# Performance work log

Hardware: AMD Instinct MI355X
Metric: run time of the kernel (lower is better)

The kernel has to match this reference:

```python
import jax, jax.numpy as jnp
import numpy as np

N_NODES = 1_000_000
N_EDGES = 16_000_000
N_FEAT = 128
NUM_GRAPHS = 8192


def setup_inputs() -> dict:
    key = jax.random.key(0)
    k_x, k_e, k_b, k_w, k_pw, k_pb = jax.random.split(key, 6)
    x = jax.random.normal(k_x, (N_NODES, N_FEAT), dtype=jnp.float32)
    edge_index = jax.random.randint(k_e, (2, N_EDGES), 0, N_NODES, dtype=jnp.int64)
    batch = jnp.sort(jax.random.randint(k_b, (N_NODES,), 0, NUM_GRAPHS, dtype=jnp.int64))
    # GCNConv lin weight (F -> 1, no bias), xavier-ish scale
    W = jax.random.normal(k_w, (N_FEAT, 1), dtype=jnp.float32) * (6.0 / (N_FEAT + 1)) ** 0.5
    # post_pool Linear(1, 1, bias=True)
    pp_w = jax.random.normal(k_pw, (1, 1), dtype=jnp.float32)
    pp_b = jax.random.normal(k_pb, (1,), dtype=jnp.float32) * 0.1
    return {"x": x, "W": W, "pp_w": pp_w, "pp_b": pp_b,
            "edge_index": edge_index, "batch": batch}


def reference(x, W, pp_w, pp_b, edge_index, batch):
    N = x.shape[0]
    h = x @ W  # [N, 1] — tiny feature after GCNConv projection
    # add self-loops (PyG GCNConv default)
    loops = jnp.arange(N, dtype=edge_index.dtype)
    src = jnp.concatenate([edge_index[0], loops])  # message sources (col j)
    dst = jnp.concatenate([edge_index[1], loops])  # aggregation targets (row i)
    # symmetric degree normalization: deg over targets incl. self-loops
    deg = jax.ops.segment_sum(jnp.ones(src.shape[0], dtype=h.dtype), dst,
                              num_segments=N)
    dinv = jnp.where(deg > 0, jax.lax.rsqrt(deg), 0.0)
    norm = dinv[src] * dinv[dst]  # [E+N]
    # gather -> normalize -> scatter-add
    agg = jax.ops.segment_sum(norm[:, None] * h[src], dst, num_segments=N)  # [N,1]
    # global_add_pool by graph id
    pooled = jax.ops.segment_sum(agg, batch, num_segments=NUM_GRAPHS)  # [G,1]
    return pooled @ pp_w.T + pp_b  # Linear(1,1)
```

## Files before the change

kernel.cpp:

```cpp
#include <hip/hip_runtime.h>
#include <hip/hip_fp16.h>

#define NUM_GRAPHS 8192
#define BSHIFT 12
#define BSIZE 4096
#define CHUNK 4096
#define NGRP 32
#define REPL 8
#define WINDOW 256
#define WPAD 257
#define FNT 512

__global__ void __launch_bounds__(256)
pair_scatter_kernel(const int* __restrict__ src, const int* __restrict__ dst,
                    int E, int nchunks, int NBUK, int capG,
                    unsigned* __restrict__ cursor, unsigned* __restrict__ slab) {
    __shared__ unsigned cnt[256];
    __shared__ unsigned lbase[256];
    __shared__ unsigned sbase[256];
    __shared__ unsigned staged[CHUNK];
    __shared__ unsigned char sbuck[CHUNK];
    __shared__ unsigned s_tot;

    const int4* s4 = (const int4*)src;
    const int4* d4 = (const int4*)dst;
    int E4 = E >> 2;
    int tid = threadIdx.x;
    int g = blockIdx.x & (NGRP - 1);

    for (int chunk = blockIdx.x; chunk < nchunks; chunk += gridDim.x) {
        cnt[tid] = 0; __syncthreads();
        int b4 = chunk * (CHUNK / 4);
        int4 vd[4], vs[4];
        unsigned short r[16];
        #pragma unroll
        for (int k = 0; k < 4; ++k) {
            int idx = b4 + k * 256 + tid;
            if (idx < E4) { vd[k] = d4[idx]; vs[k] = s4[idx]; }
            else          { vd[k] = make_int4(-1, -1, -1, -1); }
        }
        #pragma unroll
        for (int k = 0; k < 4; ++k) {
            if (vd[k].x >= 0) {
                r[4*k+0] = (unsigned short)atomicAdd(&cnt[vd[k].x >> BSHIFT], 1u);
                r[4*k+1] = (unsigned short)atomicAdd(&cnt[vd[k].y >> BSHIFT], 1u);
                r[4*k+2] = (unsigned short)atomicAdd(&cnt[vd[k].z >> BSHIFT], 1u);
                r[4*k+3] = (unsigned short)atomicAdd(&cnt[vd[k].w >> BSHIFT], 1u);
            }
        }
        __syncthreads();
        if (tid < 64) {
            unsigned run = 0;
            for (int c0 = 0; c0 < 256; c0 += 64) {
                unsigned v = cnt[c0 + tid];
                unsigned s = v;
                #pragma unroll
                for (int off = 1; off < 64; off <<= 1) {
                    unsigned o = __shfl_up(s, off);
                    if (tid >= off) s += o;
                }
                lbase[c0 + tid] = run + s - v;
                run += __shfl(s, 63);
            }
            if (tid == 0) s_tot = run;
        }
        if (tid < NBUK && cnt[tid])
            sbase[tid] = atomicAdd(&cursor[g * 256 + tid], cnt[tid]);
        __syncthreads();

        #pragma unroll
        for (int k = 0; k < 4; ++k) {
            if (vd[k].x >= 0) {
                int d0 = vd[k].x, d1 = vd[k].y, d2 = vd[k].z, d3 = vd[k].w;
                unsigned b0 = (unsigned)d0 >> BSHIFT, b1 = (unsigned)d1 >> BSHIFT;
                unsigned b2 = (unsigned)d2 >> BSHIFT, b3 = (unsigned)d3 >> BSHIFT;
                unsigned p0 = lbase[b0] + r[4*k+0];
                unsigned p1 = lbase[b1] + r[4*k+1];
                unsigned p2 = lbase[b2] + r[4*k+2];
                unsigned p3 = lbase[b3] + r[4*k+3];
                staged[p0] = ((unsigned)(d0 & (BSIZE-1)) << 20) | (unsigned)vs[k].x;
                staged[p1] = ((unsigned)(d1 & (BSIZE-1)) << 20) | (unsigned)vs[k].y;
                staged[p2] = ((unsigned)(d2 & (BSIZE-1)) << 20) | (unsigned)vs[k].z;
                staged[p3] = ((unsigned)(d3 & (BSIZE-1)) << 20) | (unsigned)vs[k].w;
                sbuck[p0] = (unsigned char)b0;
                sbuck[p1] = (unsigned char)b1;
                sbuck[p2] = (unsigned char)b2;
                sbuck[p3] = (unsigned char)b3;
            }
        }
        __syncthreads();
        unsigned tot = s_tot;
        for (unsigned pos = tid; pos < tot; pos += 256) {
            unsigned b = sbuck[pos];
            unsigned gp = sbase[b] + (pos - lbase[b]);
            if (gp < (unsigned)capG)
                slab[((size_t)g * NBUK + b) * capG + gp] = staged[pos];
        }
        __syncthreads();
    }
    if (blockIdx.x == 0 && tid < (E & 3)) {
        int i = (E & ~3) + tid;
        int d = dst[i];
        unsigned b = (unsigned)d >> BSHIFT;
        unsigned p = atomicAdd(&cursor[b], 1u);
        if (p < (unsigned)capG)
            slab[(size_t)b * capG + p] =
                ((unsigned)(d & (BSIZE-1)) << 20) | (unsigned)src[i];
    }
}

__global__ void __launch_bounds__(FNT)
hist_h_kernel(const unsigned* __restrict__ slab, int capG,
              const unsigned* __restrict__ cursor,
              unsigned* __restrict__ deg0, unsigned* __restrict__ deg1,
              const float* __restrict__ x, const float* __restrict__ W,
              float* __restrict__ h, int N, int NBUK, int nhblocks) {
    __shared__ unsigned hist[BSIZE];
    int bp = blockIdx.x, tid = threadIdx.x;

    if (bp < 2 * NBUK) {
        int b = bp >> 1, half = bp & 1;
        for (int t = tid; t < BSIZE; t += FNT) hist[t] = 0;
        __syncthreads();
        int g0 = half * 16;
        for (int gg = g0; gg < g0 + 16; gg += 8) {
            unsigned n[8], maxn = 0;
            const unsigned* sp[8];
            #pragma unroll
            for (int k = 0; k < 8; ++k) {
                unsigned nn = cursor[(gg + k) * 256 + b];
                if (nn > (unsigned)capG) nn = capG;
                n[k] = nn; if (nn > maxn) maxn = nn;
                sp[k] = slab + ((size_t)(gg + k) * NBUK + b) * capG;
            }
            for (unsigned i = tid; i < maxn; i += FNT) {
                unsigned e[8];
                #pragma unroll
                for (int k = 0; k < 8; ++k) e[k] = (i < n[k]) ? sp[k][i] : 0xFFFFFFFFu;
                #pragma unroll
                for (int k = 0; k < 8; ++k)
                    if (e[k] != 0xFFFFFFFFu) atomicAdd(&hist[e[k] >> 20], 1u);
            }
        }
        __syncthreads();
        int base = b << BSHIFT;
        int lim = N - base; if (lim > BSIZE) lim = BSIZE;
        unsigned* degP = half ? deg1 : deg0;
        for (int t = tid; t < lim; t += FNT) degP[base + t] = hist[t];
    } else {
        int hb = bp - 2 * NBUK;
        int gwave = (hb * FNT + tid) >> 6;
        int lane = tid & 63;
        int half = lane >> 5;
        int l32  = lane & 31;
        int total_waves = (nhblocks * FNT) >> 6;
        float4 wv = ((const float4*)W)[l32];
        for (int node = gwave * 2 + half; node < N; node += total_waves * 2) {
            float4 xv = ((const float4*)(x + (size_t)node * 128))[l32];
            float v = xv.x * wv.x + xv.y * wv.y + xv.z * wv.z + xv.w * wv.w;
            #pragma unroll
            for (int d = 16; d >= 1; d >>= 1) v += __shfl_xor(v, d);
            if (l32 == 0) h[node] = v;
        }
    }
}

__global__ void finalize_kernel(const float* __restrict__ h,
                                const unsigned* __restrict__ deg0,
                                const unsigned* __restrict__ deg1,
                                const int* __restrict__ batch,
                                unsigned short* __restrict__ hsh,
                                unsigned* __restrict__ pkw, int N) {
    int i = blockIdx.x * blockDim.x + threadIdx.x;
    int stride = gridDim.x * blockDim.x;
    for (; i < N; i += stride) {
        float di = rsqrtf((float)(deg0[i] + deg1[i] + 1u));
        hsh[i] = __half_as_ushort(__float2half(di * h[i]));
        pkw[i] = ((unsigned)batch[i] << 16) | __half_as_ushort(__float2half(di));
    }
}

__global__ void __launch_bounds__(512)
aggregate_kernel(const unsigned* __restrict__ slab, int capG,
                 const unsigned* __restrict__ cursor,
                 const unsigned* __restrict__ pkw,
                 const unsigned short* __restrict__ hsh,
                 float* __restrict__ pooled, int N, int NBUK) {
    __shared__ unsigned pkw_s[BSIZE];
    __shared__ float win[REPL * WPAD];
    int bp = blockIdx.x, tid = threadIdx.x;
    int b = bp >> 2, q = bp & 3;
    int base = b << BSHIFT;
    int lim = N - base; if (lim > BSIZE) lim = BSIZE;

    for (int t = tid; t < BSIZE; t += 512) pkw_s[t] = (t < lim) ? pkw[base + t] : 0u;
    for (int t = tid; t < REPL * WPAD; t += 512) win[t] = 0.0f;
    __syncthreads();
    int g_lo = (int)(pkw_s[0] >> 16);
    int g_hi = (lim > 0) ? (int)(pkw_s[lim - 1] >> 16) : g_lo;
    int width = g_hi - g_lo + 1;
    bool windowed = (width <= WINDOW);
    int r = tid & (REPL - 1);

    int n0 = q * (BSIZE / 4);
    int n1 = (q + 1) * (BSIZE / 4); if (n1 > lim) n1 = lim;
    for (int t = n0 + tid; t < n1; t += 512) {
        unsigned w = pkw_s[t];
        float di = __half2float(__ushort_as_half((unsigned short)(w & 0xFFFFu)));
        float c = di * __half2float(__ushort_as_half(hsh[base + t]));
        if (windowed) atomicAdd(&win[r * WPAD + ((w >> 16) - g_lo)], c);
        else          atomicAdd(&pooled[w >> 16], c);
    }

    int g0 = q * 8;
    unsigned n[8], maxn = 0;
    const unsigned* sp[8];
    #pragma unroll
    for (int k = 0; k < 8; ++k) {
        unsigned nn = cursor[(g0 + k) * 256 + b];
        if (nn > (unsigned)capG) nn = capG;
        n[k] = nn; if (nn > maxn) maxn = nn;
        sp[k] = slab + ((size_t)(g0 + k) * NBUK + b) * capG;
    }
    for (unsigned i = tid; i < maxn; i += 512) {
        unsigned e[8]; bool v[8];
        #pragma unroll
        for (int k = 0; k < 8; ++k) { v[k] = (i < n[k]); e[k] = v[k] ? sp[k][i] : 0u; }
        unsigned w[8];
        #pragma unroll
        for (int k = 0; k < 8; ++k) w[k] = pkw_s[e[k] >> 20];
        unsigned short hb[8];
        #pragma unroll
        for (int k = 0; k < 8; ++k) hb[k] = hsh[e[k] & 0xFFFFFu];
        #pragma unroll
        for (int k = 0; k < 8; ++k) {
            float hv = __half2float(__ushort_as_half(hb[k]));
            float di = __half2float(__ushort_as_half((unsigned short)(w[k] & 0xFFFFu)));
            float c = v[k] ? hv * di : 0.0f;
            if (windowed) atomicAdd(&win[r * WPAD + ((w[k] >> 16) - g_lo)], c);
            else if (v[k]) atomicAdd(&pooled[w[k] >> 16], c);
        }
    }
    __syncthreads();
    if (windowed) {
        for (int g = tid; g < width; g += 512) {
            float s = 0.0f;
            #pragma unroll
            for (int rr = 0; rr < REPL; ++rr) s += win[rr * WPAD + g];
            atomicAdd(&pooled[g_lo + g], s);
        }
    }
}

__global__ void out_kernel(const float* __restrict__ pooled,
                           const float* __restrict__ pp_w,
                           const float* __restrict__ pp_b,
                           float* __restrict__ out) {
    int g = blockIdx.x * blockDim.x + threadIdx.x;
    if (g < NUM_GRAPHS) out[g] = pooled[g] * pp_w[0] + pp_b[0];
}

__global__ void deg_atomic_kernel(const int* __restrict__ dst, int E,
                                  unsigned* __restrict__ deg) {
    int tid = blockIdx.x * blockDim.x + threadIdx.x;
    int stride = gridDim.x * blockDim.x;
    for (int i = tid; i < E; i += stride) atomicAdd(&deg[dst[i]], 1u);
}

__global__ void node_fb_kernel(const float* __restrict__ x,
                               const float* __restrict__ W,
                               const unsigned* __restrict__ deg,
                               const int* __restrict__ batch,
                               unsigned short* __restrict__ hsh,
                               unsigned* __restrict__ pkw, int N) {
    int gtid = blockIdx.x * blockDim.x + threadIdx.x;
    int wave = gtid >> 6;
    int lane = threadIdx.x & 63;
    int half = lane >> 5;
    int l32  = lane & 31;
    int node = wave * 2 + half;
    if (node >= N) return;
    float4 xv = ((const float4*)(x + (size_t)node * 128))[l32];
    float4 wv = ((const float4*)W)[l32];
    float v = xv.x * wv.x + xv.y * wv.y + xv.z * wv.z + xv.w * wv.w;
    #pragma unroll
    for (int d = 16; d >= 1; d >>= 1) v += __shfl_xor(v, d);
    if (l32 == 0) {
        float di = rsqrtf((float)(deg[node] + 1u));
        hsh[node] = __half_as_ushort(__float2half(di * v));
        pkw[node] = ((unsigned)batch[node] << 16) | __half_as_ushort(__float2half(di));
    }
}

__global__ void pool_self_fb_kernel(const unsigned short* __restrict__ hsh,
                                    const unsigned* __restrict__ pkw,
                                    float* __restrict__ pooled, int N) {
    int i = blockIdx.x * blockDim.x + threadIdx.x;
    if (i >= N) return;
    unsigned w = pkw[i];
    float di = __half2float(__ushort_as_half((unsigned short)(w & 0xFFFFu)));
    atomicAdd(&pooled[w >> 16], di * __half2float(__ushort_as_half(hsh[i])));
}

__global__ void __launch_bounds__(512)
edge_direct_kernel(const int* __restrict__ src, const int* __restrict__ dst, int E,
                   const unsigned short* __restrict__ hsh,
                   const unsigned* __restrict__ pkw,
                   float* __restrict__ pooled) {
    __shared__ float pool[NUM_GRAPHS];
    for (int g = threadIdx.x; g < NUM_GRAPHS; g += 512) pool[g] = 0.0f;
    __syncthreads();
    int tid = blockIdx.x * 512 + threadIdx.x;
    int stride = gridDim.x * 512;
    for (int i = tid; i < E; i += stride) {
        unsigned w = pkw[dst[i]];
        float c = __half2float(__ushort_as_half(hsh[src[i]])) *
                  __half2float(__ushort_as_half((unsigned short)(w & 0xFFFFu)));
        atomicAdd(&pool[w >> 16], c);
    }
    __syncthreads();
    for (int g = threadIdx.x; g < NUM_GRAPHS; g += 512)
        if (pool[g] != 0.0f) atomicAdd(&pooled[g], pool[g]);
}

extern "C" void kernel_launch(void* const* d_in, const int* in_sizes, int n_in,
                              void* d_out, int out_size, void* d_ws, size_t ws_size,
                              hipStream_t stream) {
    const float* x    = (const float*)d_in[0];
    const float* W    = (const float*)d_in[1];
    const float* pp_w = (const float*)d_in[2];
    const float* pp_b = (const float*)d_in[3];
    const int*   ei   = (const int*)d_in[4];
    const int*   batch= (const int*)d_in[5];
    float* out = (float*)d_out;

    const int E = in_sizes[4] / 2;
    const int N = in_sizes[5];
    const int* src = ei;
    const int* dst = ei + E;
    int NBUK = (N + BSIZE - 1) >> BSHIFT;
    int nchunks = (E + CHUNK - 1) / CHUNK;

    char* ws = (char*)d_ws;
    size_t off = 0;
    auto alloc = [&](size_t bytes) {
        size_t o = off; off = (off + bytes + 255) & ~(size_t)255; return o;
    };
    size_t zero_bytes = (size_t)NUM_GRAPHS * 4 + (size_t)NGRP * 256 * 4;
    size_t zero_off   = alloc(zero_bytes);
    float*    pooled = (float*)(ws + zero_off);
    unsigned* cursor = (unsigned*)(ws + zero_off + (size_t)NUM_GRAPHS * 4);

    size_t h_off    = alloc((size_t)N * 4);
    size_t deg0_off = alloc((size_t)N * 4);
    size_t deg1_off = alloc((size_t)N * 4);
    size_t hsh_off  = alloc((size_t)N * 2);
    size_t pkw_off  = alloc((size_t)N * 4);

    int meanG = E / (NBUK * NGRP) + 1;
    int capG = (meanG + meanG / 8 + 512 + 3) & ~3;
    size_t slab_off = alloc((size_t)NGRP * NBUK * (size_t)capG * 4);

    bool fast_ok = (NBUK <= 256) && (N <= (1 << 20)) && (off <= ws_size);

    float*          h    = (float*)(ws + h_off);
    unsigned*       deg0 = (unsigned*)(ws + deg0_off);
    unsigned*       deg1 = (unsigned*)(ws + deg1_off);
    unsigned short* hsh  = (unsigned short*)(ws + hsh_off);
    unsigned*       pkw  = (unsigned*)(ws + pkw_off);
    unsigned*       slab = (unsigned*)(ws + slab_off);

    hipMemsetAsync(ws + zero_off, 0, zero_bytes, stream);

    if (fast_ok) {
        int grid = nchunks < 4096 ? nchunks : 4096;
        pair_scatter_kernel<<<grid, 256, 0, stream>>>(src, dst, E, nchunks, NBUK,
                                                      capG, cursor, slab);
        int nhblocks = 2048;
        hist_h_kernel<<<2 * NBUK + nhblocks, FNT, 0, stream>>>(
            slab, capG, cursor, deg0, deg1, x, W, h, N, NBUK, nhblocks);
        finalize_kernel<<<1024, 256, 0, stream>>>(h, deg0, deg1, batch, hsh, pkw, N);
        aggregate_kernel<<<4 * NBUK, 512, 0, stream>>>(slab, capG, cursor, pkw,
                                                       hsh, pooled, N, NBUK);
    } else {
        hipMemsetAsync(deg0, 0, (size_t)N * 4, stream);
        deg_atomic_kernel<<<2048, 256, 0, stream>>>(dst, E, deg0);
        int node_blocks = (N + 7) / 8;
        node_fb_kernel<<<node_blocks, 256, 0, stream>>>(x, W, deg0, batch, hsh, pkw, N);
        pool_self_fb_kernel<<<(N + 255) / 256, 256, 0, stream>>>(hsh, pkw, pooled, N);
        edge_direct_kernel<<<512, 512, 0, stream>>>(src, dst, E, hsh, pkw, pooled);
    }

    out_kernel<<<(NUM_GRAPHS + 255) / 256, 256, 0, stream>>>(pooled, pp_w, pp_b, out);
}
```

Baseline: 276.2 us.

## Split h projection across scatter and histogram kernels to overlap memory work

The first half of the node projection h = x·W moves into the edge scatter kernel. Even block indices do the edge bucketing and odd ones compute h for the first N/2 nodes, and the histogram kernel now handles only the rest. The aim is to overlap the bandwidth-heavy read of x with the atomic-bound scatter, balancing the two kernels. The scatter grid falls from 4096 to 2048 blocks, which may lengthen the scatter phase.

```diff
diff --git a/kernel.cpp b/kernel.cpp
--- a/kernel.cpp
+++ b/kernel.cpp
@@ -10,11 +10,15 @@
 #define WINDOW 256
 #define WPAD 257
 #define FNT 512
+#define SGRID 2048
+#define HGRID1 2048
 
 __global__ void __launch_bounds__(256)
-pair_scatter_kernel(const int* __restrict__ src, const int* __restrict__ dst,
-                    int E, int nchunks, int NBUK, int capG,
-                    unsigned* __restrict__ cursor, unsigned* __restrict__ slab) {
+scatter_h_kernel(const int* __restrict__ src, const int* __restrict__ dst,
+                 int E, int nchunks, int NBUK, int capG,
+                 unsigned* __restrict__ cursor, unsigned* __restrict__ slab,
+                 const float* __restrict__ x, const float* __restrict__ W,
+                 float* __restrict__ h, int Nh) {
     __shared__ unsigned cnt[256];
     __shared__ unsigned lbase[256];
     __shared__ unsigned sbase[256];
@@ -22,90 +26,110 @@
     __shared__ unsigned char sbuck[CHUNK];
     __shared__ unsigned s_tot;
 
-    const int4* s4 = (const int4*)src;
-    const int4* d4 = (const int4*)dst;
-    int E4 = E >> 2;
+    int bid = blockIdx.x;
     int tid = threadIdx.x;
-    int g = blockIdx.x & (NGRP - 1);
-
-    for (int chunk = blockIdx.x; chunk < nchunks; chunk += gridDim.x) {
-        cnt[tid] = 0; __syncthreads();
-        int b4 = chunk * (CHUNK / 4);
-        int4 vd[4], vs[4];
-        unsigned short r[16];
-        #pragma unroll
-        for (int k = 0; k < 4; ++k) {
-            int idx = b4 + k * 256 + tid;
-            if (idx < E4) { vd[k] = d4[idx]; vs[k] = s4[idx]; }
-            else          { vd[k] = make_int4(-1, -1, -1, -1); }
-        }
-        #pragma unroll
-        for (int k = 0; k < 4; ++k) {
-            if (vd[k].x >= 0) {
-                r[4*k+0] = (unsigned short)atomicAdd(&cnt[vd[k].x >> BSHIFT], 1u);
-                r[4*k+1] = (unsigned short)atomicAdd(&cnt[vd[k].y >> BSHIFT], 1u);
-                r[4*k+2] = (unsigned short)atomicAdd(&cnt[vd[k].z >> BSHIFT], 1u);
-                r[4*k+3] = (unsigned short)atomicAdd(&cnt[vd[k].w >> BSHIFT], 1u);
-            }
-        }
-        __syncthreads();
-        if (tid < 64) {
-            unsigned run = 0;
-            for (int c0 = 0; c0 < 256; c0 += 64) {
-                unsigned v = cnt[c0 + tid];
-                unsigned s = v;
-                #pragma unroll
-                for (int off = 1; off < 64; off <<= 1) {
-                    unsigned o = __shfl_up(s, off);
-                    if (tid >= off) s += o;
+
+    if ((bid & 1) == 0) {
+        int sid = bid >> 1;
+        const int4* s4 = (const int4*)src;
+        const int4* d4 = (const int4*)dst;
+        int E4 = E >> 2;
+        int g = sid & (NGRP - 1);
+
+        for (int chunk = sid; chunk < nchunks; chunk += SGRID) {
+            cnt[tid] = 0; __syncthreads();
+            int b4 = chunk * (CHUNK / 4);
+            int4 vd[4], vs[4];
+            unsigned short r[16];
+            #pragma unroll
+            for (int k = 0; k < 4; ++k) {
+                int idx = b4 + k * 256 + tid;
+                if (idx < E4) { vd[k] = d4[idx]; vs[k] = s4[idx]; }
+                else          { vd[k] = make_int4(-1, -1, -1, -1); }
+            }
+            #pragma unroll
+            for (int k = 0; k < 4; ++k) {
+                if (vd[k].x >= 0) {
+                    r[4*k+0] = (unsigned short)atomicAdd(&cnt[vd[k].x >> BSHIFT], 1u);
+                    r[4*k+1] = (unsigned short)atomicAdd(&cnt[vd[k].y >> BSHIFT], 1u);
+                    r[4*k+2] = (unsigned short)atomicAdd(&cnt[vd[k].z >> BSHIFT], 1u);
+                    r[4*k+3] = (unsigned short)atomicAdd(&cnt[vd[k].w >> BSHIFT], 1u);
                 }
-                lbase[c0 + tid] = run + s - v;
-                run += __shfl(s, 63);
-            }
-            if (tid == 0) s_tot = run;
-        }
-        if (tid < NBUK && cnt[tid])
-            sbase[tid] = atomicAdd(&cursor[g * 256 + tid], cnt[tid]);
-        __syncthreads();
-
-        #pragma unroll
-        for (int k = 0; k < 4; ++k) {
-            if (vd[k].x >= 0) {
-                int d0 = vd[k].x, d1 = vd[k].y, d2 = vd[k].z, d3 = vd[k].w;
-                unsigned b0 = (unsigned)d0 >> BSHIFT, b1 = (unsigned)d1 >> BSHIFT;
-                unsigned b2 = (unsigned)d2 >> BSHIFT, b3 = (unsigned)d3 >> BSHIFT;
-                unsigned p0 = lbase[b0] + r[4*k+0];
-                unsigned p1 = lbase[b1] + r[4*k+1];
-                unsigned p2 = lbase[b2] + r[4*k+2];
-                unsigned p3 = lbase[b3] + r[4*k+3];
-                staged[p0] = ((unsigned)(d0 & (BSIZE-1)) << 20) | (unsigned)vs[k].x;
-                staged[p1] = ((unsigned)(d1 & (BSIZE-1)) << 20) | (unsigned)vs[k].y;
-                staged[p2] = ((unsigned)(d2 & (BSIZE-1)) << 20) | (unsigned)vs[k].z;
-                staged[p3] = ((unsigned)(d3 & (BSIZE-1)) << 20) | (unsigned)vs[k].w;
-                sbuck[p0] = (unsigned char)b0;
-                sbuck[p1] = (unsigned char)b1;
-                sbuck[p2] = (unsigned char)b2;
-                sbuck[p3] = (unsigned char)b3;
-            }
-        }
-        __syncthreads();
-        unsigned tot = s_tot;
-        for (unsigned pos = tid; pos < tot; pos += 256) {
-            unsigned b = sbuck[pos];
-            unsigned gp = sbase[b] + (pos - lbase[b]);
-            if (gp < (unsigned)capG)
-                slab[((size_t)g * NBUK + b) * capG + gp] = staged[pos];
-        }
-        __syncthreads();
-    }
-    if (blockIdx.x == 0 && tid < (E & 3)) {
-        int i = (E & ~3) + tid;
-        int d = dst[i];
-        unsigned b = (unsigned)d >> BSHIFT;
-        unsigned p = atomicAdd(&cursor[b], 1u);
-        if (p < (unsigned)capG)
-            slab[(size_t)b * capG + p] =
-                ((unsigned)(d & (BSIZE-1)) << 20) | (unsigned)src[i];
+            }
+            __syncthreads();
+            if (tid < 64) {
+                unsigned run = 0;
+                for (int c0 = 0; c0 < 256; c0 += 64) {
+                    unsigned v = cnt[c0 + tid];
+                    unsigned s = v;
+                    #pragma unroll
+                    for (int off = 1; off < 64; off <<= 1) {
+                        unsigned o = __shfl_up(s, off);
+                        if (tid >= off) s += o;
+                    }
+                    lbase[c0 + tid] = run + s - v;
+                    run += __shfl(s, 63);
+                }
+                if (tid == 0) s_tot = run;
+            }
+            if (tid < NBUK && cnt[tid])
+                sbase[tid] = atomicAdd(&cursor[g * 256 + tid], cnt[tid]);
+            __syncthreads();
+
+            #pragma unroll
+            for (int k = 0; k < 4; ++k) {
+                if (vd[k].x >= 0) {
+                    int d0 = vd[k].x, d1 = vd[k].y, d2 = vd[k].z, d3 = vd[k].w;
+                    unsigned b0 = (unsigned)d0 >> BSHIFT, b1 = (unsigned)d1 >> BSHIFT;
+                    unsigned b2 = (unsigned)d2 >> BSHIFT, b3 = (unsigned)d3 >> BSHIFT;
+                    unsigned p0 = lbase[b0] + r[4*k+0];
+                    unsigned p1 = lbase[b1] + r[4*k+1];
+                    unsigned p2 = lbase[b2] + r[4*k+2];
+                    unsigned p3 = lbase[b3] + r[4*k+3];
+                    staged[p0] = ((unsigned)(d0 & (BSIZE-1)) << 20) | (unsigned)vs[k].x;
+                    staged[p1] = ((unsigned)(d1 & (BSIZE-1)) << 20) | (unsigned)vs[k].y;
+                    staged[p2] = ((unsigned)(d2 & (BSIZE-1)) << 20) | (unsigned)vs[k].z;
+                    staged[p3] = ((unsigned)(d3 & (BSIZE-1)) << 20) | (unsigned)vs[k].w;
+                    sbuck[p0] = (unsigned char)b0;
+                    sbuck[p1] = (unsigned char)b1;
+                    sbuck[p2] = (unsigned char)b2;
+                    sbuck[p3] = (unsigned char)b3;
+                }
+            }
+            __syncthreads();
+            unsigned tot = s_tot;
+            for (unsigned pos = tid; pos < tot; pos += 256) {
+                unsigned b = sbuck[pos];
+                unsigned gp = sbase[b] + (pos - lbase[b]);
+                if (gp < (unsigned)capG)
+                    slab[((size_t)g * NBUK + b) * capG + gp] = staged[pos];
+            }
+            __syncthreads();
+        }
+        if (sid == 0 && tid < (E & 3)) {
+            int i = (E & ~3) + tid;
+            int d = dst[i];
+            unsigned b = (unsigned)d >> BSHIFT;
+            unsigned p = atomicAdd(&cursor[b], 1u);
+            if (p < (unsigned)capG)
+                slab[(size_t)b * capG + p] =
+                    ((unsigned)(d & (BSIZE-1)) << 20) | (unsigned)src[i];
+        }
+    } else {
+        int hid = bid >> 1;
+        int gwave = (hid * 256 + tid) >> 6;
+        int lane = tid & 63;
+        int half = lane >> 5;
+        int l32  = lane & 31;
+        int total_waves = (HGRID1 * 256) >> 6;
+        float4 wv = ((const float4*)W)[l32];
+        for (int node = gwave * 2 + half; node < Nh; node += total_waves * 2) {
+            float4 xv = ((const float4*)(x + (size_t)node * 128))[l32];
+            float v = xv.x * wv.x + xv.y * wv.y + xv.z * wv.z + xv.w * wv.w;
+            #pragma unroll
+            for (int d = 16; d >= 1; d >>= 1) v += __shfl_xor(v, d);
+            if (l32 == 0) h[node] = v;
+        }
     }
 }
 
@@ -114,7 +138,7 @@
               const unsigned* __restrict__ cursor,
               unsigned* __restrict__ deg0, unsigned* __restrict__ deg1,
               const float* __restrict__ x, const float* __restrict__ W,
-              float* __restrict__ h, int N, int NBUK, int nhblocks) {
+              float* __restrict__ h, int Nh, int N, int NBUK, int nhblocks) {
     __shared__ unsigned hist[BSIZE];
     int bp = blockIdx.x, tid = threadIdx.x;
 
@@ -155,7 +179,7 @@
         int l32  = lane & 31;
         int total_waves = (nhblocks * FNT) >> 6;
         float4 wv = ((const float4*)W)[l32];
-        for (int node = gwave * 2 + half; node < N; node += total_waves * 2) {
+        for (int node = Nh + gwave * 2 + half; node < N; node += total_waves * 2) {
             float4 xv = ((const float4*)(x + (size_t)node * 128))[l32];
             float v = xv.x * wv.x + xv.y * wv.y + xv.z * wv.z + xv.w * wv.w;
             #pragma unroll
@@ -373,12 +397,12 @@
     hipMemsetAsync(ws + zero_off, 0, zero_bytes, stream);
 
     if (fast_ok) {
-        int grid = nchunks < 4096 ? nchunks : 4096;
-        pair_scatter_kernel<<<grid, 256, 0, stream>>>(src, dst, E, nchunks, NBUK,
-                                                      capG, cursor, slab);
+        int Nh = N >> 1;
+        scatter_h_kernel<<<SGRID + HGRID1, 256, 0, stream>>>(
+            src, dst, E, nchunks, NBUK, capG, cursor, slab, x, W, h, Nh);
         int nhblocks = 2048;
         hist_h_kernel<<<2 * NBUK + nhblocks, FNT, 0, stream>>>(
-            slab, capG, cursor, deg0, deg1, x, W, h, N, NBUK, nhblocks);
+            slab, capG, cursor, deg0, deg1, x, W, h, Nh, N, NBUK, nhblocks);
         finalize_kernel<<<1024, 256, 0, stream>>>(h, deg0, deg1, batch, hsh, pkw, N);
         aggregate_kernel<<<4 * NBUK, 512, 0, stream>>>(slab, capG, cursor, pkw,
                                                        hsh, pooled, N, NBUK);
```

Result: faster. 270.6 us (median of 2 runs) (-2.0%).
